# Optimization experiments

Hardware: AMD Instinct MI355X
Metric: run time of the kernel (lower is better)

## Reference

```python
import jax, jax.numpy as jnp
import numpy as np

N_SVC, N_POD, N_NODE = 2000, 8000, 1000
T, F, H = 32, 64, 128
E_SVC, E_IN, E_NI = 30000, 24000, 24000


def setup_inputs() -> dict:
    key = jax.random.key(0)
    ks = jax.random.split(key, 32)
    s = 0.05
    inp = {
        'feat_svc': jax.random.normal(ks[0], (N_SVC, T, F), jnp.float32),
        'feat_pod': jax.random.normal(ks[1], (N_POD, T, F), jnp.float32),
        'feat_node': jax.random.normal(ks[2], (N_NODE, T, F), jnp.float32),
        # per-timestep GraphConv weights (one HGraphConvLayer per window step)
        'w_svc': jax.random.normal(ks[3], (T, F, H), jnp.float32) * s,
        'b_svc': jnp.zeros((T, H), jnp.float32),
        'w_in': jax.random.normal(ks[4], (T, F, H), jnp.float32) * s,   # pod -> node
        'b_in': jnp.zeros((T, H), jnp.float32),
        'w_ni': jax.random.normal(ks[5], (T, F, H), jnp.float32) * s,   # node -> pod
        'b_ni': jnp.zeros((T, H), jnp.float32),
        # per-timestep output linears (hidden -> 1) per node type
        'lw_svc': jax.random.normal(ks[6], (T, H), jnp.float32) * s,
        'lb_svc': jnp.zeros((T,), jnp.float32),
        'lw_pod': jax.random.normal(ks[7], (T, H), jnp.float32) * s,
        'lb_pod': jnp.zeros((T,), jnp.float32),
        'lw_node': jax.random.normal(ks[8], (T, H), jnp.float32) * s,
        'lb_node': jnp.zeros((T,), jnp.float32),
        # 2-layer LSTM (input_size = T = window_simple_size)
        'w_ih0': jax.random.normal(ks[9], (4 * H, T), jnp.float32) * s,
        'w_hh0': jax.random.normal(ks[10], (4 * H, H), jnp.float32) * s,
        'b_ih0': jnp.zeros((4 * H,), jnp.float32),
        'b_hh0': jnp.zeros((4 * H,), jnp.float32),
        'w_ih1': jax.random.normal(ks[11], (4 * H, H), jnp.float32) * s,
        'w_hh1': jax.random.normal(ks[12], (4 * H, H), jnp.float32) * s,
        'b_ih1': jnp.zeros((4 * H,), jnp.float32),
        'b_hh1': jnp.zeros((4 * H,), jnp.float32),
        # heterograph edge lists
        'e_svc_src': jax.random.randint(ks[13], (E_SVC,), 0, N_SVC, jnp.int64),
        'e_svc_dst': jax.random.randint(ks[14], (E_SVC,), 0, N_SVC, jnp.int64),
        'e_in_src': jax.random.randint(ks[15], (E_IN,), 0, N_POD, jnp.int64),
        'e_in_dst': jax.random.randint(ks[16], (E_IN,), 0, N_NODE, jnp.int64),
        'e_ni_src': jax.random.randint(ks[17], (E_NI,), 0, N_NODE, jnp.int64),
        'e_ni_dst': jax.random.randint(ks[18], (E_NI,), 0, N_POD, jnp.int64),
    }
    return inp


def _graph_conv(x, src, dst, n_dst, w, b):
    # DGL GraphConv, norm='both', batched over all T timesteps at once.
    # x: [N_src, T, F], w: [T, F, H], b: [T, H] -> [N_dst, T, H]
    n_src = x.shape[0]
    ones_e = jnp.ones(src.shape[0], x.dtype)
    out_deg = jnp.clip(jax.ops.segment_sum(ones_e, src, num_segments=n_src), 1.0)
    in_deg = jnp.clip(jax.ops.segment_sum(ones_e, dst, num_segments=n_dst), 1.0)
    xs = x * (out_deg ** -0.5)[:, None, None]
    agg = jax.ops.segment_sum(xs[src], dst, num_segments=n_dst)   # [N_dst, T, F]
    agg = agg * (in_deg ** -0.5)[:, None, None]
    return jnp.einsum('ntf,tfh->nth', agg, w) + b[None]


def _leaky(v):
    return jnp.where(v >= 0, v, 0.01 * v)


def _lstm(x, w_ih, w_hh, b_ih, b_hh):
    # unbatched LSTM over leading (node) axis; PyTorch gate order i,f,g,o
    Hh = w_hh.shape[1]
    b = b_ih + b_hh
    def step(carry, xt):
        h, c = carry
        g = xt @ w_ih.T + h @ w_hh.T + b
        i, f, gg, o = jnp.split(g, 4)
        i = jax.nn.sigmoid(i); f = jax.nn.sigmoid(f)
        gg = jnp.tanh(gg); o = jax.nn.sigmoid(o)
        c = f * c + i * gg
        h = o * jnp.tanh(c)
        return (h, c), h
    init = (jnp.zeros((Hh,), x.dtype), jnp.zeros((Hh,), x.dtype))
    _, ys = jax.lax.scan(step, init, x)
    return ys


def _forward(feat_svc, feat_pod, feat_node,
             w_svc, b_svc, w_in, b_in, w_ni, b_ni,
             lw_svc, lb_svc, lw_pod, lb_pod, lw_node, lb_node,
             w_ih0, w_hh0, b_ih0, b_hh0, w_ih1, w_hh1, b_ih1, b_hh1,
             e_svc_src, e_svc_dst, e_in_src, e_in_dst, e_ni_src, e_ni_dst):
    # HeteroGraphConv (sum aggregate; each dst type receives one edge type)
    h_svc = _graph_conv(feat_svc, e_svc_src, e_svc_dst, feat_svc.shape[0], w_svc, b_svc)
    h_node = _graph_conv(feat_pod, e_in_src, e_in_dst, feat_node.shape[0], w_in, b_in)
    h_pod = _graph_conv(feat_node, e_ni_src, e_ni_dst, feat_pod.shape[0], w_ni, b_ni)
    # per-timestep LeakyReLU + Linear(hidden -> 1), per node type
    s_svc = jnp.einsum('nth,th->nt', _leaky(h_svc), lw_svc) + lb_svc[None]
    s_pod = jnp.einsum('nth,th->nt', _leaky(h_pod), lw_pod) + lb_pod[None]
    s_node = jnp.einsum('nth,th->nt', _leaky(h_node), lw_node) + lb_node[None]
    x_seq = jnp.concatenate([s_svc, s_pod, s_node], axis=0)   # [N_total, T]
    # 2-layer LSTM over the node axis, input_size = T
    y = _lstm(x_seq, w_ih0, w_hh0, b_ih0, b_hh0)
    y = _lstm(y, w_ih1, w_hh1, b_ih1, b_hh1)
    return y   # [N_total, H]


def reference(feat_svc, feat_pod, feat_node,
              w_svc, b_svc, w_in, b_in, w_ni, b_ni,
              lw_svc, lb_svc, lw_pod, lb_pod, lw_node, lb_node,
              w_ih0, w_hh0, b_ih0, b_hh0, w_ih1, w_hh1, b_ih1, b_hh1,
              e_svc_src, e_svc_dst, e_in_src, e_in_dst, e_ni_src, e_ni_dst):
    return _forward(feat_svc, feat_pod, feat_node,
                    w_svc, b_svc, w_in, b_in, w_ni, b_ni,
                    lw_svc, lb_svc, lw_pod, lb_pod, lw_node, lb_node,
                    w_ih0, w_hh0, b_ih0, b_hh0, w_ih1, w_hh1, b_ih1, b_hh1,
                    e_svc_src, e_svc_dst, e_in_src, e_in_dst, e_ni_src, e_ni_dst)
```

## Files before the change

### kernel.cpp

```cpp
#include <hip/hip_runtime.h>

#define NSVC 2000
#define NPOD 8000
#define NNODE 1000
#define NTOT 11000
#define TT 32
#define FF 64
#define HH 128
#define EA 30000
#define EB 24000
#define EC 24000
#define CHK 64
#define NCH ((NTOT + CHK - 1) / CHK)

__device__ __forceinline__ float ld_agent(const float* p) {
    return __hip_atomic_load(p, __ATOMIC_RELAXED, __HIP_MEMORY_SCOPE_AGENT);
}
__device__ __forceinline__ void st_agent(float* p, float v) {
    __hip_atomic_store(p, v, __ATOMIC_RELAXED, __HIP_MEMORY_SCOPE_AGENT);
}
__device__ __forceinline__ void bar_fast() {
    asm volatile("s_waitcnt lgkmcnt(0)" ::: "memory");
    __builtin_amdgcn_s_barrier();
}

__global__ void k_count(const int* __restrict__ src, const int* __restrict__ dst, int E,
                        float* oc, float* ic) {
    int e = blockIdx.x * 256 + threadIdx.x;
    if (e < E) {
        atomicAdd(oc + src[e], 1.f);
        atomicAdd(ic + dst[e], 1.f);
    }
}

__global__ void k_scan(const float* cA, int nA, int* oA,
                       const float* cB, int nB, int* oB,
                       const float* cC, int nC, int* oC) {
    const float* c; int n; int* o;
    if (blockIdx.x == 0)      { c = cA; n = nA; o = oA; }
    else if (blockIdx.x == 1) { c = cB; n = nB; o = oB; }
    else                      { c = cC; n = nC; o = oC; }
    __shared__ int s[256];
    __shared__ int carry;
    int tid = threadIdx.x;
    if (tid == 0) { carry = 0; o[0] = 0; }
    __syncthreads();
    for (int base = 0; base < n; base += 256) {
        int idx = base + tid;
        int v = (idx < n) ? (int)c[idx] : 0;
        s[tid] = v;
        __syncthreads();
        for (int d = 1; d < 256; d <<= 1) {
            int t = (tid >= d) ? s[tid - d] : 0;
            __syncthreads();
            s[tid] += t;
            __syncthreads();
        }
        if (idx < n) o[idx + 1] = carry + s[tid];
        __syncthreads();
        if (tid == 255) carry += s[255];
        __syncthreads();
    }
}

__global__ void k_scatter(const int* __restrict__ src, const int* __restrict__ dst, int E,
                          const int* __restrict__ off, int* cur, int* csr) {
    int e = blockIdx.x * 256 + threadIdx.x;
    if (e < E) {
        int d = dst[e];
        int p = atomicAdd(cur + d, 1);
        csr[off[d] + p] = src[e];
    }
}

__global__ __launch_bounds__(256) void k_conv(
    const float* __restrict__ x,
    const float* __restrict__ w,
    const float* __restrict__ b,
    const float* __restrict__ lw,
    const float* __restrict__ lb,
    const float* __restrict__ oc,
    const float* __restrict__ ic,
    const int* __restrict__ off, const int* __restrict__ csr,
    float* __restrict__ xseq, int Ndst, int rowofs)
{
    __shared__ float wl[FF * HH];
    __shared__ float bl[HH], lwl[HH];
    __shared__ float accs[4][FF];
    int t = blockIdx.x;
    int tid = threadIdx.x;
    for (int i = tid; i < FF * HH; i += 256) wl[i] = w[t * FF * HH + i];
    if (tid < HH) { bl[tid] = b[t * HH + tid]; lwl[tid] = lw[t * HH + tid]; }
    int wv = tid >> 6, lane = tid & 63;
    int dstn = blockIdx.y * 4 + wv;
    __syncthreads();
    if (dstn < Ndst) {
        float a = 0.f;
        int e0 = off[dstn], e1 = off[dstn + 1];
        for (int i = e0; i < e1; ++i) {
            int s = csr[i];
            float xs = x[(size_t)s * (TT * FF) + t * FF + lane];
            a += xs * rsqrtf(fmaxf(oc[s], 1.f));
        }
        a *= rsqrtf(fmaxf(ic[dstn], 1.f));
        accs[wv][lane] = a;
    }
    __syncthreads();
    if (dstn < Ndst) {
        float h0 = bl[lane], h1v = bl[64 + lane];
        #pragma unroll
        for (int f = 0; f < FF; ++f) {
            float af = accs[wv][f];
            h0  += af * wl[f * HH + lane];
            h1v += af * wl[f * HH + 64 + lane];
        }
        h0  = (h0  >= 0.f) ? h0  : 0.01f * h0;
        h1v = (h1v >= 0.f) ? h1v : 0.01f * h1v;
        float p = h0 * lwl[lane] + h1v * lwl[64 + lane];
        #pragma unroll
        for (int o2 = 32; o2 >= 1; o2 >>= 1) p += __shfl_down(p, o2);
        if (lane == 0) xseq[(size_t)(rowofs + dstn) * TT + t] = p + lb[t];
    }
}

__global__ __launch_bounds__(256) void k_proj(
    const float* __restrict__ xin, int K,
    const float* __restrict__ wih,
    const float* __restrict__ bih, const float* __restrict__ bhh,
    float* __restrict__ Xout, int N)
{
    __shared__ float xt[16 * 128];
    int n0 = blockIdx.x * 16, tid = threadIdx.x;
    for (int i = tid; i < 16 * K; i += 256) {
        int nn = i / K, kk = i - nn * K;
        int n = n0 + nn;
        xt[i] = (n < N) ? xin[(size_t)n * K + kk] : 0.f;
    }
    __syncthreads();
    float acc0[16], acc1[16];
    #pragma unroll
    for (int i = 0; i < 16; ++i) { acc0[i] = 0.f; acc1[i] = 0.f; }
    int r0 = tid, r1 = tid + 256;
    for (int k = 0; k < K; ++k) {
        float w0 = wih[(size_t)r0 * K + k];
        float w1 = wih[(size_t)r1 * K + k];
        #pragma unroll
        for (int i = 0; i < 16; ++i) {
            float xv = xt[i * K + k];
            acc0[i] += xv * w0;
            acc1[i] += xv * w1;
        }
    }
    float b0 = bih[r0] + bhh[r0], b1 = bih[r1] + bhh[r1];
    for (int i = 0; i < 16; ++i) {
        int n = n0 + i;
        if (n < N) {
            Xout[(size_t)n * 512 + r0] = acc0[i] + b0;
            Xout[(size_t)n * 512 + r1] = acc1[i] + b1;
        }
    }
}

__device__ void lstm_rec(const float* __restrict__ X, const float* __restrict__ Whh,
                         float* __restrict__ Hout, bool agent_x, bool agent_h,
                         int* wflag, int* sflag)
{
    __shared__ __align__(16) float hb[2][4 * 36];
    const int tid = threadIdx.x;
    const int j = tid >> 2, p = tid & 3;
    float w[4][32];
    #pragma unroll
    for (int g = 0; g < 4; ++g) {
        const float4* wr = reinterpret_cast<const float4*>(Whh + (size_t)(g * HH + j) * HH + p * 32);
        #pragma unroll
        for (int k4 = 0; k4 < 8; ++k4) {
            float4 v = wr[k4];
            w[g][4*k4+0] = v.x; w[g][4*k4+1] = v.y;
            w[g][4*k4+2] = v.z; w[g][4*k4+3] = v.w;
        }
    }
    if (tid < HH) hb[0][(tid >> 5) * 36 + (tid & 31)] = 0.f;
    const float k1 = (p == 2) ? -2.f : 1.f;
    const float k2 = (p == 2) ? 2.f : -1.f;
    const float k3 = (p == 2) ? 1.f : 0.f;
    float c = 0.f;
    int cur = 0;
    __syncthreads();
    for (int ch = 0; ch < NCH; ++ch) {
        const int n0 = ch * CHK;
        const int n1 = (n0 + CHK < NTOT) ? (n0 + CHK) : NTOT;
        if (wflag) {
            if (tid == 0) {
                while (__hip_atomic_load(wflag + ch, __ATOMIC_RELAXED, __HIP_MEMORY_SCOPE_AGENT) == 0)
                    __builtin_amdgcn_s_sleep(2);
            }
            __syncthreads();
            __threadfence();
        }
        const float* xp = X + (size_t)n0 * 512 + p * HH + j;
        float xcur = agent_x ? ld_agent(xp) : xp[0];
        float xn1 = (n0 + 1 < n1) ? (agent_x ? ld_agent(xp + 512) : xp[512]) : 0.f;
        for (int n = n0; n < n1; ++n) {
            float xn2 = 0.f;
            if (n + 2 < n1) {
                const float* q = xp + (size_t)(n + 2 - n0) * 512;
                xn2 = agent_x ? ld_agent(q) : q[0];
            }
            const float4* hr = reinterpret_cast<const float4*>(&hb[cur][p * 36]);
            float h[32];
            #pragma unroll
            for (int k4 = 0; k4 < 8; ++k4) {
                float4 v4 = hr[k4];
                h[4*k4+0] = v4.x; h[4*k4+1] = v4.y;
                h[4*k4+2] = v4.z; h[4*k4+3] = v4.w;
            }
            float s0 = 0.f, s1 = 0.f, s2 = 0.f, s3 = 0.f;
            #pragma unroll
            for (int k = 0; k < 32; ++k) {
                float hv = h[k];
                s0 = fmaf(w[0][k], hv, s0);
                s1 = fmaf(w[1][k], hv, s1);
                s2 = fmaf(w[2][k], hv, s2);
                s3 = fmaf(w[3][k], hv, s3);
            }
            float zA = (p & 1) ? s0 : s1;
            float rA = __shfl_xor(zA, 1);
            float u  = ((p & 1) ? s1 : s0) + rA;
            float zB = (p & 1) ? s2 : s3;
            float rB = __shfl_xor(zB, 1);
            float v  = ((p & 1) ? s3 : s2) + rB;
            float zC = (p & 2) ? u : v;
            float rC = __shfl_xor(zC, 2);
            float sf = (((p & 2) ? v : u) + rC) + xcur;
            float e = __expf(k2 * sf);
            float a = fmaf(k1, __builtin_amdgcn_rcpf(1.f + e), k3);
            float af = __shfl_xor(a, 1);
            float ag = __shfl_xor(a, 2);
            float ao = __shfl_xor(a, 3);
            c = fmaf(af, c, a * ag);
            float e2 = __expf(2.f * c);
            float th = fmaf(-2.f, __builtin_amdgcn_rcpf(1.f + e2), 1.f);
            float hnew = ao * th;
            if (p == 0) {
                hb[cur ^ 1][(j >> 5) * 36 + (j & 31)] = hnew;
                if (agent_h) st_agent(Hout + (size_t)n * HH + j, hnew);
                else         Hout[(size_t)n * HH + j] = hnew;
            }
            bar_fast();
            cur ^= 1;
            xcur = xn1; xn1 = xn2;
        }
        if (sflag) {
            __syncthreads();
            if (tid == 0)
                __hip_atomic_store(sflag + ch, 1, __ATOMIC_RELEASE, __HIP_MEMORY_SCOPE_AGENT);
        }
    }
}

__device__ void proj_work(const float* __restrict__ h1, const float* __restrict__ Wih,
                          const float* __restrict__ bih, const float* __restrict__ bhh,
                          float* __restrict__ X2, int* wflag, int* sflag)
{
    __shared__ float hl[CHK * HH];
    const int tid = threadIdx.x;
    const float bsum = bih[tid] + bhh[tid];
    const float4* wr = reinterpret_cast<const float4*>(Wih + (size_t)tid * HH);
    for (int ch = 0; ch < NCH; ++ch) {
        const int n0 = ch * CHK;
        const int cnt = (n0 + CHK < NTOT) ? CHK : (NTOT - n0);
        if (tid == 0) {
            while (__hip_atomic_load(wflag + ch, __ATOMIC_RELAXED, __HIP_MEMORY_SCOPE_AGENT) == 0)
                __builtin_amdgcn_s_sleep(2);
        }
        __syncthreads();
        __threadfence();
        for (int i = tid; i < cnt * HH; i += 512)
            hl[i] = ld_agent(h1 + (size_t)n0 * HH + i);
        __syncthreads();
        for (int t0 = 0; t0 < cnt; t0 += 16) {
            float acc[16];
            #pragma unroll
            for (int i = 0; i < 16; ++i) acc[i] = bsum;
            for (int k4 = 0; k4 < HH / 4; ++k4) {
                float4 wv = wr[k4];
                #pragma unroll
                for (int i = 0; i < 16; ++i) {
                    const float* hh = &hl[(t0 + i) * HH + 4 * k4];
                    acc[i] += wv.x*hh[0] + wv.y*hh[1] + wv.z*hh[2] + wv.w*hh[3];
                }
            }
            int tl = cnt - t0; if (tl > 16) tl = 16;
            for (int i = 0; i < tl; ++i)
                st_agent(X2 + (size_t)(n0 + t0 + i) * 512 + tid, acc[i]);
        }
        __syncthreads();
        if (tid == 0)
            __hip_atomic_store(sflag + ch, 1, __ATOMIC_RELEASE, __HIP_MEMORY_SCOPE_AGENT);
    }
}

__global__ __launch_bounds__(512) void k_pipe(
    const float* __restrict__ X1, const float* __restrict__ w_hh0, float* __restrict__ h1,
    const float* __restrict__ w_ih1, const float* __restrict__ b_ih1, const float* __restrict__ b_hh1,
    float* __restrict__ X2, const float* __restrict__ w_hh1, float* __restrict__ out,
    int* flags1, int* flags2)
{
    if (blockIdx.x == 0)
        lstm_rec(X1, w_hh0, h1, false, true, nullptr, flags1);
    else if (blockIdx.x == 1)
        proj_work(h1, w_ih1, b_ih1, b_hh1, X2, flags1, flags2);
    else
        lstm_rec(X2, w_hh1, out, true, false, flags2, nullptr);
}

extern "C" void kernel_launch(void* const* d_in, const int* in_sizes, int n_in,
                              void* d_out, int out_size, void* d_ws, size_t ws_size,
                              hipStream_t stream) {
    const float* feat_svc = (const float*)d_in[0];
    const float* feat_pod = (const float*)d_in[1];
    const float* feat_node= (const float*)d_in[2];
    const float* w_svc = (const float*)d_in[3];
    const float* b_svc = (const float*)d_in[4];
    const float* w_in  = (const float*)d_in[5];
    const float* b_in  = (const float*)d_in[6];
    const float* w_ni  = (const float*)d_in[7];
    const float* b_ni  = (const float*)d_in[8];
    const float* lw_svc = (const float*)d_in[9];
    const float* lb_svc = (const float*)d_in[10];
    const float* lw_pod = (const float*)d_in[11];
    const float* lb_pod = (const float*)d_in[12];
    const float* lw_node= (const float*)d_in[13];
    const float* lb_node= (const float*)d_in[14];
    const float* w_ih0 = (const float*)d_in[15];
    const float* w_hh0 = (const float*)d_in[16];
    const float* b_ih0 = (const float*)d_in[17];
    const float* b_hh0 = (const float*)d_in[18];
    const float* w_ih1 = (const float*)d_in[19];
    const float* w_hh1 = (const float*)d_in[20];
    const float* b_ih1 = (const float*)d_in[21];
    const float* b_hh1 = (const float*)d_in[22];
    const int* eA_src = (const int*)d_in[23];
    const int* eA_dst = (const int*)d_in[24];
    const int* eB_src = (const int*)d_in[25];
    const int* eB_dst = (const int*)d_in[26];
    const int* eC_src = (const int*)d_in[27];
    const int* eC_dst = (const int*)d_in[28];

    float* ws = (float*)d_ws;
    float* ocA = ws + 0;
    float* icA = ws + 2000;
    float* ocB = ws + 4000;
    float* icB = ws + 12000;
    float* ocC = ws + 13000;
    float* icC = ws + 14000;
    int* curA = (int*)(ws + 22000);
    int* curB = (int*)(ws + 24000);
    int* curC = (int*)(ws + 25000);
    int* offA = (int*)(ws + 33000);
    int* offB = (int*)(ws + 35001);
    int* offC = (int*)(ws + 36002);
    int* sA   = (int*)(ws + 44003);
    int* sB   = (int*)(ws + 74003);
    int* sC   = (int*)(ws + 98003);
    float* xseq = ws + 122003;
    float* X1   = ws + 474003;
    float* h1   = ws + 6106003;
    int* flags1 = (int*)(ws + 7514003);
    int* flags2 = flags1 + NCH;
    float* X2   = X1;

    hipMemsetAsync(d_ws, 0, 33000 * sizeof(float), stream);
    hipMemsetAsync(flags1, 0, 2 * NCH * sizeof(int), stream);

    k_count<<<(EA + 255) / 256, 256, 0, stream>>>(eA_src, eA_dst, EA, ocA, icA);
    k_count<<<(EB + 255) / 256, 256, 0, stream>>>(eB_src, eB_dst, EB, ocB, icB);
    k_count<<<(EC + 255) / 256, 256, 0, stream>>>(eC_src, eC_dst, EC, ocC, icC);

    k_scan<<<3, 256, 0, stream>>>(icA, NSVC, offA, icB, NNODE, offB, icC, NPOD, offC);

    k_scatter<<<(EA + 255) / 256, 256, 0, stream>>>(eA_src, eA_dst, EA, offA, curA, sA);
    k_scatter<<<(EB + 255) / 256, 256, 0, stream>>>(eB_src, eB_dst, EB, offB, curB, sB);
    k_scatter<<<(EC + 255) / 256, 256, 0, stream>>>(eC_src, eC_dst, EC, offC, curC, sC);

    k_conv<<<dim3(TT, (NSVC + 3) / 4), 256, 0, stream>>>(
        feat_svc, w_svc, b_svc, lw_svc, lb_svc, ocA, icA, offA, sA, xseq, NSVC, 0);
    k_conv<<<dim3(TT, (NPOD + 3) / 4), 256, 0, stream>>>(
        feat_node, w_ni, b_ni, lw_pod, lb_pod, ocC, icC, offC, sC, xseq, NPOD, NSVC);
    k_conv<<<dim3(TT, (NNODE + 3) / 4), 256, 0, stream>>>(
        feat_pod, w_in, b_in, lw_node, lb_node, ocB, icB, offB, sB, xseq, NNODE, NSVC + NPOD);

    k_proj<<<(NTOT + 15) / 16, 256, 0, stream>>>(xseq, TT, w_ih0, b_ih0, b_hh0, X1, NTOT);

    k_pipe<<<3, 512, 0, stream>>>(X1, w_hh0, h1, w_ih1, b_ih1, b_hh1,
                                  X2, w_hh1, (float*)d_out, flags1, flags2);
}
```

Measured before the change: 10.30 ms.

## Merge per-type graph kernels and restructure LSTM recurrence to full-row weights

```diff
diff --git a/kernel.cpp b/kernel.cpp
--- a/kernel.cpp
+++ b/kernel.cpp
@@ -10,6 +10,7 @@
 #define EA 30000
 #define EB 24000
 #define EC 24000
+#define ETOT (EA + EB + EC)
 #define CHK 64
 #define NCH ((NTOT + CHK - 1) / CHK)
 
@@ -24,12 +25,20 @@
     __builtin_amdgcn_s_barrier();
 }
 
-__global__ void k_count(const int* __restrict__ src, const int* __restrict__ dst, int E,
-                        float* oc, float* ic) {
+__global__ void k_count3(const int* __restrict__ sA, const int* __restrict__ dA,
+                         const int* __restrict__ sB, const int* __restrict__ dB,
+                         const int* __restrict__ sC, const int* __restrict__ dC,
+                         float* ocA, float* icA, float* ocB, float* icB,
+                         float* ocC, float* icC) {
     int e = blockIdx.x * 256 + threadIdx.x;
-    if (e < E) {
-        atomicAdd(oc + src[e], 1.f);
-        atomicAdd(ic + dst[e], 1.f);
+    if (e < EA) {
+        atomicAdd(ocA + sA[e], 1.f); atomicAdd(icA + dA[e], 1.f);
+    } else if (e < EA + EB) {
+        int i = e - EA;
+        atomicAdd(ocB + sB[i], 1.f); atomicAdd(icB + dB[i], 1.f);
+    } else if (e < ETOT) {
+        int i = e - EA - EB;
+        atomicAdd(ocC + sC[i], 1.f); atomicAdd(icC + dC[i], 1.f);
     }
 }
 
@@ -63,44 +72,82 @@
     }
 }
 
-__global__ void k_scatter(const int* __restrict__ src, const int* __restrict__ dst, int E,
-                          const int* __restrict__ off, int* cur, int* csr) {
+__global__ void k_scatter3(const int* __restrict__ sA, const int* __restrict__ dA,
+                           const int* __restrict__ sB, const int* __restrict__ dB,
+                           const int* __restrict__ sC, const int* __restrict__ dC,
+                           const int* offA, int* curA, int* csrA,
+                           const int* offB, int* curB, int* csrB,
+                           const int* offC, int* curC, int* csrC) {
     int e = blockIdx.x * 256 + threadIdx.x;
-    if (e < E) {
-        int d = dst[e];
-        int p = atomicAdd(cur + d, 1);
-        csr[off[d] + p] = src[e];
-    }
-}
-
-__global__ __launch_bounds__(256) void k_conv(
-    const float* __restrict__ x,
-    const float* __restrict__ w,
-    const float* __restrict__ b,
-    const float* __restrict__ lw,
-    const float* __restrict__ lb,
-    const float* __restrict__ oc,
-    const float* __restrict__ ic,
-    const int* __restrict__ off, const int* __restrict__ csr,
-    float* __restrict__ xseq, int Ndst, int rowofs)
+    if (e < EA) {
+        int d = dA[e]; int p = atomicAdd(curA + d, 1); csrA[offA[d] + p] = sA[e];
+    } else if (e < EA + EB) {
+        int i = e - EA;
+        int d = dB[i]; int p = atomicAdd(curB + d, 1); csrB[offB[d] + p] = sB[i];
+    } else if (e < ETOT) {
+        int i = e - EA - EB;
+        int d = dC[i]; int p = atomicAdd(curC + d, 1); csrC[offC[d] + p] = sC[i];
+    }
+}
+
+#define YA ((NSVC + 3) / 4)
+#define YC ((NPOD + 3) / 4)
+#define YB ((NNODE + 3) / 4)
+__global__ __launch_bounds__(256) void k_conv3(
+    const float* __restrict__ feat_svc, const float* __restrict__ feat_pod,
+    const float* __restrict__ feat_node,
+    const float* __restrict__ w_svc, const float* __restrict__ b_svc,
+    const float* __restrict__ lw_svc, const float* __restrict__ lb_svc,
+    const float* __restrict__ w_ni, const float* __restrict__ b_ni,
+    const float* __restrict__ lw_pod, const float* __restrict__ lb_pod,
+    const float* __restrict__ w_in, const float* __restrict__ b_in,
+    const float* __restrict__ lw_node, const float* __restrict__ lb_node,
+    const float* ocA, const float* icA, const int* offA, const int* csrA,
+    const float* ocC, const float* icC, const int* offC, const int* csrC,
+    const float* ocB, const float* icB, const int* offB, const int* csrB,
+    float* __restrict__ xseq)
 {
     __shared__ float wl[FF * HH];
     __shared__ float bl[HH], lwl[HH];
     __shared__ float accs[4][FF];
-    int t = blockIdx.x;
-    int tid = threadIdx.x;
+    const int t = blockIdx.x;
+    const int tid = threadIdx.x;
+    int yb = blockIdx.y;
+    const float *x, *w, *b, *lw, *lb, *oc, *ic; const int *off, *csr;
+    int Ndst, rowofs;
+    if (yb < YA) {
+        x = feat_svc; w = w_svc; b = b_svc; lw = lw_svc; lb = lb_svc;
+        oc = ocA; ic = icA; off = offA; csr = csrA; Ndst = NSVC; rowofs = 0;
+    } else if (yb < YA + YC) {
+        yb -= YA;
+        x = feat_node; w = w_ni; b = b_ni; lw = lw_pod; lb = lb_pod;
+        oc = ocC; ic = icC; off = offC; csr = csrC; Ndst = NPOD; rowofs = NSVC;
+    } else {
+        yb -= YA + YC;
+        x = feat_pod; w = w_in; b = b_in; lw = lw_node; lb = lb_node;
+        oc = ocB; ic = icB; off = offB; csr = csrB; Ndst = NNODE; rowofs = NSVC + NPOD;
+    }
     for (int i = tid; i < FF * HH; i += 256) wl[i] = w[t * FF * HH + i];
     if (tid < HH) { bl[tid] = b[t * HH + tid]; lwl[tid] = lw[t * HH + tid]; }
-    int wv = tid >> 6, lane = tid & 63;
-    int dstn = blockIdx.y * 4 + wv;
+    const int wv = tid >> 6, lane = tid & 63;
+    const int dstn = yb * 4 + wv;
     __syncthreads();
     if (dstn < Ndst) {
         float a = 0.f;
-        int e0 = off[dstn], e1 = off[dstn + 1];
+        const int e0 = off[dstn], e1 = off[dstn + 1];
+        const float* xb = x + (size_t)t * FF + lane;
+        float xsP = 0.f, ocP = 1.f;
+        if (e0 < e1) {
+            int s0 = csr[e0];
+            xsP = xb[(size_t)s0 * (TT * FF)]; ocP = oc[s0];
+        }
         for (int i = e0; i < e1; ++i) {
-            int s = csr[i];
-            float xs = x[(size_t)s * (TT * FF) + t * FF + lane];
-            a += xs * rsqrtf(fmaxf(oc[s], 1.f));
+            float xs = xsP, od = ocP;
+            if (i + 1 < e1) {
+                int s2 = csr[i + 1];
+                xsP = xb[(size_t)s2 * (TT * FF)]; ocP = oc[s2];
+            }
+            a = fmaf(xs, rsqrtf(fmaxf(od, 1.f)), a);
         }
         a *= rsqrtf(fmaxf(ic[dstn], 1.f));
         accs[wv][lane] = a;
@@ -111,8 +158,8 @@
         #pragma unroll
         for (int f = 0; f < FF; ++f) {
             float af = accs[wv][f];
-            h0  += af * wl[f * HH + lane];
-            h1v += af * wl[f * HH + 64 + lane];
+            h0  = fmaf(af, wl[f * HH + lane], h0);
+            h1v = fmaf(af, wl[f * HH + 64 + lane], h1v);
         }
         h0  = (h0  >= 0.f) ? h0  : 0.01f * h0;
         h1v = (h1v >= 0.f) ? h1v : 0.01f * h1v;
@@ -122,6 +169,8 @@
         if (lane == 0) xseq[(size_t)(rowofs + dstn) * TT + t] = p + lb[t];
     }
 }
+
+__device__ __forceinline__ int xcol(int r) { return ((r & 127) << 2) | (r >> 7); }
 
 __global__ __launch_bounds__(256) void k_proj(
     const float* __restrict__ xin, int K,
@@ -147,16 +196,17 @@
         #pragma unroll
         for (int i = 0; i < 16; ++i) {
             float xv = xt[i * K + k];
-            acc0[i] += xv * w0;
-            acc1[i] += xv * w1;
+            acc0[i] = fmaf(xv, w0, acc0[i]);
+            acc1[i] = fmaf(xv, w1, acc1[i]);
         }
     }
     float b0 = bih[r0] + bhh[r0], b1 = bih[r1] + bhh[r1];
+    int c0 = xcol(r0), c1 = xcol(r1);
     for (int i = 0; i < 16; ++i) {
         int n = n0 + i;
         if (n < N) {
-            Xout[(size_t)n * 512 + r0] = acc0[i] + b0;
-            Xout[(size_t)n * 512 + r1] = acc1[i] + b1;
+            Xout[(size_t)n * 512 + c0] = acc0[i] + b0;
+            Xout[(size_t)n * 512 + c1] = acc1[i] + b1;
         }
     }
 }
@@ -165,90 +215,85 @@
                          float* __restrict__ Hout, bool agent_x, bool agent_h,
                          int* wflag, int* sflag)
 {
-    __shared__ __align__(16) float hb[2][4 * 36];
+    __shared__ __align__(16) float hb0s[HH], hb1s[HH];
     const int tid = threadIdx.x;
-    const int j = tid >> 2, p = tid & 3;
-    float w[4][32];
-    #pragma unroll
-    for (int g = 0; g < 4; ++g) {
-        const float4* wr = reinterpret_cast<const float4*>(Whh + (size_t)(g * HH + j) * HH + p * 32);
+    const int j = tid >> 2, g = tid & 3;
+    const bool g0 = (g == 0);
+    const int lbase = (tid & 63) & ~3;
+    float w[HH];
+    {
+        const float4* wr = reinterpret_cast<const float4*>(Whh + (size_t)(g * HH + j) * HH);
         #pragma unroll
-        for (int k4 = 0; k4 < 8; ++k4) {
+        for (int k4 = 0; k4 < 32; ++k4) {
             float4 v = wr[k4];
-            w[g][4*k4+0] = v.x; w[g][4*k4+1] = v.y;
-            w[g][4*k4+2] = v.z; w[g][4*k4+3] = v.w;
-        }
-    }
-    if (tid < HH) hb[0][(tid >> 5) * 36 + (tid & 31)] = 0.f;
-    const float k1 = (p == 2) ? -2.f : 1.f;
-    const float k2 = (p == 2) ? 2.f : -1.f;
-    const float k3 = (p == 2) ? 1.f : 0.f;
+            w[4*k4+0] = v.x; w[4*k4+1] = v.y; w[4*k4+2] = v.z; w[4*k4+3] = v.w;
+        }
+    }
+    if (tid < HH) hb0s[tid] = 0.f;
+    const float k1 = (g == 2) ? -2.f : 1.f;
+    const float k2 = (g == 2) ? 2.f : -1.f;
+    const float k3 = (g == 2) ? 1.f : 0.f;
     float c = 0.f;
-    int cur = 0;
     __syncthreads();
+
+    auto step = [&](const float* hsrc, float* hdst, float xc, float* ho) {
+        const float4* hr = reinterpret_cast<const float4*>(hsrc);
+        float s0 = 0.f, s1 = 0.f, s2 = 0.f, s3 = 0.f;
+        #pragma unroll
+        for (int q = 0; q < 8; ++q) {
+            float4 h0 = hr[q], h1 = hr[8+q], h2 = hr[16+q], h3 = hr[24+q];
+            s0 = fmaf(w[4*q+0],  h0.x, s0); s0 = fmaf(w[4*q+1],  h0.y, s0);
+            s0 = fmaf(w[4*q+2],  h0.z, s0); s0 = fmaf(w[4*q+3],  h0.w, s0);
+            s1 = fmaf(w[32+4*q+0], h1.x, s1); s1 = fmaf(w[32+4*q+1], h1.y, s1);
+            s1 = fmaf(w[32+4*q+2], h1.z, s1); s1 = fmaf(w[32+4*q+3], h1.w, s1);
+            s2 = fmaf(w[64+4*q+0], h2.x, s2); s2 = fmaf(w[64+4*q+1], h2.y, s2);
+            s2 = fmaf(w[64+4*q+2], h2.z, s2); s2 = fmaf(w[64+4*q+3], h2.w, s2);
+            s3 = fmaf(w[96+4*q+0], h3.x, s3); s3 = fmaf(w[96+4*q+1], h3.y, s3);
+            s3 = fmaf(w[96+4*q+2], h3.z, s3); s3 = fmaf(w[96+4*q+3], h3.w, s3);
+        }
+        float sf = ((s0 + s1) + (s2 + s3)) + xc;
+        float ev = __expf(k2 * sf);
+        float a = fmaf(k1, __builtin_amdgcn_rcpf(1.f + ev), k3);
+        float ai  = __shfl(a, lbase);
+        float af_ = __shfl(a, lbase + 1);
+        float agg = __shfl(a, lbase + 2);
+        float ao_ = __shfl(a, lbase + 3);
+        c = fmaf(af_, c, ai * agg);
+        float e2 = __expf(2.f * c);
+        float th = fmaf(-2.f, __builtin_amdgcn_rcpf(1.f + e2), 1.f);
+        float hnew = ao_ * th;
+        if (g0) {
+            hdst[j] = hnew;
+            if (agent_h) st_agent(ho, hnew); else *ho = hnew;
+        }
+        bar_fast();
+    };
+
     for (int ch = 0; ch < NCH; ++ch) {
         const int n0 = ch * CHK;
         const int n1 = (n0 + CHK < NTOT) ? (n0 + CHK) : NTOT;
         if (wflag) {
             if (tid == 0) {
                 while (__hip_atomic_load(wflag + ch, __ATOMIC_RELAXED, __HIP_MEMORY_SCOPE_AGENT) == 0)
-                    __builtin_amdgcn_s_sleep(2);
+                    __builtin_amdgcn_s_sleep(1);
             }
             __syncthreads();
             __threadfence();
         }
-        const float* xp = X + (size_t)n0 * 512 + p * HH + j;
-        float xcur = agent_x ? ld_agent(xp) : xp[0];
-        float xn1 = (n0 + 1 < n1) ? (agent_x ? ld_agent(xp + 512) : xp[512]) : 0.f;
-        for (int n = n0; n < n1; ++n) {
-            float xn2 = 0.f;
+        const float* xb = X + tid;
+        float xc0 = agent_x ? ld_agent(xb + (size_t)n0 * 512) : xb[(size_t)n0 * 512];
+        float xc1 = agent_x ? ld_agent(xb + (size_t)(n0+1) * 512) : xb[(size_t)(n0+1) * 512];
+        for (int n = n0; n < n1; n += 2) {
+            float xp2 = 0.f, xp3 = 0.f;
             if (n + 2 < n1) {
-                const float* q = xp + (size_t)(n + 2 - n0) * 512;
-                xn2 = agent_x ? ld_agent(q) : q[0];
+                const float* q2 = xb + (size_t)(n + 2) * 512;
+                const float* q3 = xb + (size_t)(n + 3) * 512;
+                xp2 = agent_x ? ld_agent(q2) : q2[0];
+                xp3 = agent_x ? ld_agent(q3) : q3[0];
             }
-            const float4* hr = reinterpret_cast<const float4*>(&hb[cur][p * 36]);
-            float h[32];
-            #pragma unroll
-            for (int k4 = 0; k4 < 8; ++k4) {
-                float4 v4 = hr[k4];
-                h[4*k4+0] = v4.x; h[4*k4+1] = v4.y;
-                h[4*k4+2] = v4.z; h[4*k4+3] = v4.w;
-            }
-            float s0 = 0.f, s1 = 0.f, s2 = 0.f, s3 = 0.f;
-            #pragma unroll
-            for (int k = 0; k < 32; ++k) {
-                float hv = h[k];
-                s0 = fmaf(w[0][k], hv, s0);
-                s1 = fmaf(w[1][k], hv, s1);
-                s2 = fmaf(w[2][k], hv, s2);
-                s3 = fmaf(w[3][k], hv, s3);
-            }
-            float zA = (p & 1) ? s0 : s1;
-            float rA = __shfl_xor(zA, 1);
-            float u  = ((p & 1) ? s1 : s0) + rA;
-            float zB = (p & 1) ? s2 : s3;
-            float rB = __shfl_xor(zB, 1);
-            float v  = ((p & 1) ? s3 : s2) + rB;
-            float zC = (p & 2) ? u : v;
-            float rC = __shfl_xor(zC, 2);
-            float sf = (((p & 2) ? v : u) + rC) + xcur;
-            float e = __expf(k2 * sf);
-            float a = fmaf(k1, __builtin_amdgcn_rcpf(1.f + e), k3);
-            float af = __shfl_xor(a, 1);
-            float ag = __shfl_xor(a, 2);
-            float ao = __shfl_xor(a, 3);
-            c = fmaf(af, c, a * ag);
-            float e2 = __expf(2.f * c);
-            float th = fmaf(-2.f, __builtin_amdgcn_rcpf(1.f + e2), 1.f);
-            float hnew = ao * th;
-            if (p == 0) {
-                hb[cur ^ 1][(j >> 5) * 36 + (j & 31)] = hnew;
-                if (agent_h) st_agent(Hout + (size_t)n * HH + j, hnew);
-                else         Hout[(size_t)n * HH + j] = hnew;
-            }
-            bar_fast();
-            cur ^= 1;
-            xcur = xn1; xn1 = xn2;
+            step(hb0s, hb1s, xc0, Hout + (size_t)n * HH + j);
+            step(hb1s, hb0s, xc1, Hout + (size_t)(n + 1) * HH + j);
+            xc0 = xp2; xc1 = xp3;
         }
         if (sflag) {
             __syncthreads();
@@ -265,13 +310,14 @@
     __shared__ float hl[CHK * HH];
     const int tid = threadIdx.x;
     const float bsum = bih[tid] + bhh[tid];
+    const int col = xcol(tid);
     const float4* wr = reinterpret_cast<const float4*>(Wih + (size_t)tid * HH);
     for (int ch = 0; ch < NCH; ++ch) {
         const int n0 = ch * CHK;
         const int cnt = (n0 + CHK < NTOT) ? CHK : (NTOT - n0);
         if (tid == 0) {
             while (__hip_atomic_load(wflag + ch, __ATOMIC_RELAXED, __HIP_MEMORY_SCOPE_AGENT) == 0)
-                __builtin_amdgcn_s_sleep(2);
+                __builtin_amdgcn_s_sleep(1);
         }
         __syncthreads();
         __threadfence();
@@ -292,7 +338,7 @@
             }
             int tl = cnt - t0; if (tl > 16) tl = 16;
             for (int i = 0; i < tl; ++i)
-                st_agent(X2 + (size_t)(n0 + t0 + i) * 512 + tid, acc[i]);
+                st_agent(X2 + (size_t)(n0 + t0 + i) * 512 + col, acc[i]);
         }
         __syncthreads();
         if (tid == 0)
@@ -300,7 +346,7 @@
     }
 }
 
-__global__ __launch_bounds__(512) void k_pipe(
+__global__ __launch_bounds__(512, 2) void k_pipe(
     const float* __restrict__ X1, const float* __restrict__ w_hh0, float* __restrict__ h1,
     const float* __restrict__ w_ih1, const float* __restrict__ b_ih1, const float* __restrict__ b_hh1,
     float* __restrict__ X2, const float* __restrict__ w_hh1, float* __restrict__ out,
@@ -373,22 +419,25 @@
     hipMemsetAsync(d_ws, 0, 33000 * sizeof(float), stream);
     hipMemsetAsync(flags1, 0, 2 * NCH * sizeof(int), stream);
 
-    k_count<<<(EA + 255) / 256, 256, 0, stream>>>(eA_src, eA_dst, EA, ocA, icA);
-    k_count<<<(EB + 255) / 256, 256, 0, stream>>>(eB_src, eB_dst, EB, ocB, icB);
-    k_count<<<(EC + 255) / 256, 256, 0, stream>>>(eC_src, eC_dst, EC, ocC, icC);
+    k_count3<<<(ETOT + 255) / 256, 256, 0, stream>>>(
+        eA_src, eA_dst, eB_src, eB_dst, eC_src, eC_dst,
+        ocA, icA, ocB, icB, ocC, icC);
 
     k_scan<<<3, 256, 0, stream>>>(icA, NSVC, offA, icB, NNODE, offB, icC, NPOD, offC);
 
-    k_scatter<<<(EA + 255) / 256, 256, 0, stream>>>(eA_src, eA_dst, EA, offA, curA, sA);
-    k_scatter<<<(EB + 255) / 256, 256, 0, stream>>>(eB_src, eB_dst, EB, offB, curB, sB);
-    k_scatter<<<(EC + 255) / 256, 256, 0, stream>>>(eC_src, eC_dst, EC, offC, curC, sC);
-
-    k_conv<<<dim3(TT, (NSVC + 3) / 4), 256, 0, stream>>>(
-        feat_svc, w_svc, b_svc, lw_svc, lb_svc, ocA, icA, offA, sA, xseq, NSVC, 0);
-    k_conv<<<dim3(TT, (NPOD + 3) / 4), 256, 0, stream>>>(
-        feat_node, w_ni, b_ni, lw_pod, lb_pod, ocC, icC, offC, sC, xseq, NPOD, NSVC);
-    k_conv<<<dim3(TT, (NNODE + 3) / 4), 256, 0, stream>>>(
-        feat_pod, w_in, b_in, lw_node, lb_node, ocB, icB, offB, sB, xseq, NNODE, NSVC + NPOD);
+    k_scatter3<<<(ETOT + 255) / 256, 256, 0, stream>>>(
+        eA_src, eA_dst, eB_src, eB_dst, eC_src, eC_dst,
+        offA, curA, sA, offB, curB, sB, offC, curC, sC);
+
+    k_conv3<<<dim3(TT, YA + YC + YB), 256, 0, stream>>>(
+        feat_svc, feat_pod, feat_node,
+        w_svc, b_svc, lw_svc, lb_svc,
+        w_ni, b_ni, lw_pod, lb_pod,
+        w_in, b_in, lw_node, lb_node,
+        ocA, icA, offA, sA,
+        ocC, icC, offC, sC,
+        ocB, icB, offB, sB,
+        xseq);
 
     k_proj<<<(NTOT + 15) / 16, 256, 0, stream>>>(xseq, TT, w_ih0, b_ih0, b_hh0, X1, NTOT);
 
```

Measured after the change: 13.56 ms. 31.6% more time.
